# Performance work log

Hardware: AMD Instinct MI355X
Metric: run time of the kernel (lower is better)

Reference implementation:

```python
import jax, jax.numpy as jnp
import numpy as np

NUM_HEADS = 2
DIM_NODE = 100
DIM_EDGE = 100
DIM_TIME = 100
DIM_OUT = 100
N_DST = 32768
N_EDGE = 524288
LN_EPS = 1e-5


def setup_inputs() -> dict:
    key = jax.random.key(0)
    ks = jax.random.split(key, 12)
    dst_h = jax.random.normal(ks[0], (N_DST, DIM_NODE), dtype=jnp.float32)
    src_h = jax.random.normal(ks[1], (N_EDGE, DIM_NODE), dtype=jnp.float32)
    efeat = jax.random.normal(ks[2], (N_EDGE, DIM_EDGE), dtype=jnp.float32)
    # time deltas are non-negative elapsed times
    time_deltas = jax.random.uniform(ks[3], (N_EDGE,), dtype=jnp.float32) * 1000.0
    edge_dst = jnp.sort(jax.random.randint(ks[4], (N_EDGE,), 0, N_DST, dtype=jnp.int32))
    # TimeEncode: fixed geometric frequencies, zero bias
    time_w = jnp.asarray(1.0 / 10 ** np.linspace(0, 9, DIM_TIME), dtype=jnp.float32)
    time_b = jnp.zeros((DIM_TIME,), dtype=jnp.float32)
    def lin(k, fan_out, fan_in):
        s = 1.0 / np.sqrt(fan_in)
        return jax.random.uniform(k, (fan_out, fan_in), jnp.float32, -s, s)
    wq_w = lin(ks[5], DIM_OUT, DIM_NODE + DIM_TIME)
    wq_b = jax.random.normal(ks[6], (DIM_OUT,), jnp.float32) * 0.02
    wkv_w = lin(ks[7], 2 * DIM_OUT, DIM_NODE + DIM_EDGE + DIM_TIME)
    wkv_b = jax.random.normal(ks[8], (2 * DIM_OUT,), jnp.float32) * 0.02
    wout_w = lin(ks[9], DIM_OUT, DIM_NODE + DIM_OUT)
    wout_b = jax.random.normal(ks[10], (DIM_OUT,), jnp.float32) * 0.02
    ln_g = jnp.ones((DIM_OUT,), jnp.float32)
    ln_b = jnp.zeros((DIM_OUT,), jnp.float32)
    return dict(dst_h=dst_h, src_h=src_h, efeat=efeat, time_deltas=time_deltas,
                edge_dst=edge_dst, time_w=time_w, time_b=time_b,
                wq_w=wq_w, wq_b=wq_b, wkv_w=wkv_w, wkv_b=wkv_b,
                wout_w=wout_w, wout_b=wout_b, ln_g=ln_g, ln_b=ln_b)


def reference(dst_h, src_h, efeat, time_deltas, edge_dst, time_w, time_b,
              wq_w, wq_b, wkv_w, wkv_b, wout_w, wout_b, ln_g, ln_b):
    n_dst = dst_h.shape[0]
    dim_out = wq_w.shape[0]
    dh = dim_out // NUM_HEADS
    # TimeEncode: cos(w*t + b); zero-time feature for dst nodes
    zero_tf = jnp.broadcast_to(jnp.cos(time_b), (n_dst, time_b.shape[0]))
    nbr_tf = jnp.cos(time_deltas[:, None] * time_w[None, :] + time_b)  # [E, dim_time]
    Q = jnp.concatenate([dst_h, zero_tf], axis=1) @ wq_w.T + wq_b       # [N_dst, dim_out]
    Z = jnp.concatenate([src_h, efeat, nbr_tf], axis=1) @ wkv_w.T + wkv_b  # [E, 2*dim_out]
    K = Z[:, :dim_out].reshape(-1, NUM_HEADS, dh)
    V = Z[:, dim_out:].reshape(-1, NUM_HEADS, dh)
    Qe = Q[edge_dst].reshape(-1, NUM_HEADS, dh)  # edge_view gather
    attn = jnp.sum(Qe * K, axis=2)               # [E, H]
    attn = jax.nn.leaky_relu(attn, negative_slope=0.2)
    # edge_softmax: segment softmax over edges grouped by dst
    m = jax.ops.segment_max(attn, edge_dst, num_segments=n_dst)
    e = jnp.exp(attn - m[edge_dst])
    s = jax.ops.segment_sum(e, edge_dst, num_segments=n_dst)
    a = e / s[edge_dst]                           # [E, H]
    out_e = (V * a[:, :, None]).reshape(-1, dim_out)
    out = jax.ops.segment_sum(out_e, edge_dst, num_segments=n_dst)  # edge_reduce sum
    out = jnp.concatenate([out, dst_h], axis=1) @ wout_w.T + wout_b
    out = jax.nn.relu(out)  # dropout disabled (eval)
    mu = jnp.mean(out, axis=-1, keepdims=True)
    var = jnp.var(out, axis=-1, keepdims=True)
    return (out - mu) / jnp.sqrt(var + LN_EPS) * ln_g + ln_b
```

## Files before the change

### kernel.cpp

```cpp
#include <hip/hip_runtime.h>
#include <math.h>

#define N_DST   32768
#define N_EDGE  524288
#define LN_EPS  1e-5f

typedef __attribute__((ext_vector_type(8))) short short8b;
typedef __attribute__((ext_vector_type(4))) float f32x4;

static __device__ __forceinline__ unsigned short f2bf(float f) {
    unsigned u = __float_as_uint(f);
    u += 0x7fff + ((u >> 16) & 1);
    return (unsigned short)(u >> 16);
}

__global__ void k_prep(const float* __restrict__ wkv_w, const float* __restrict__ wq_w,
                       const float* __restrict__ wq_b, const float* __restrict__ time_b,
                       const float* __restrict__ wout_w,
                       float* __restrict__ zq, float* __restrict__ wout_t,
                       unsigned short* __restrict__ Bv) {
    int idx = blockIdx.x * 256 + threadIdx.x;
    if (idx < 100) {
        float acc = wq_b[idx];
        for (int j = 0; j < 100; ++j)
            acc += cosf(time_b[j]) * wq_w[idx * 200 + 100 + j];
        zq[idx] = acc;
    } else if (idx < 20100) {
        int r = idx - 100;
        wout_t[r] = wout_w[(size_t)(r % 100) * 200 + r / 100];
    } else if (idx < 95364) {
        int r2 = idx - 20100;
        int jj = r2 & 7, l = (r2 >> 3) & 63, nf = (r2 >> 9) % 7, kc = r2 / 3584;
        int j = kc * 32 + ((l >> 4) << 3) + jj;
        int o = nf * 16 + (l & 15);
        float v = (j < 600 && o < 100 && (j / 300 == o / 50))
                  ? wkv_w[(size_t)(100 + o) * 300 + (j % 300)] : 0.f;
        Bv[r2] = f2bf(v);
    }
}

__global__ void k_precomp(const float* __restrict__ wq_w, const float* __restrict__ wkv_w,
                          const float* __restrict__ wkv_b, const float* __restrict__ zq,
                          float* __restrict__ A2, float* __restrict__ C2) {
    int idx = blockIdx.x * 256 + threadIdx.x;
    if (idx < 60200) {
        int i = idx / 602, j = idx % 602;
        float acc = 0.f;
        if (j < 600) {
            int h = j / 300, cc = j % 300;
            const float* __restrict__ wq = wq_w + (size_t)(h * 50) * 200 + i;
            const float* __restrict__ wk = wkv_w + (size_t)(h * 50) * 300 + cc;
            #pragma unroll 10
            for (int d = 0; d < 50; ++d)
                acc = fmaf(wq[(size_t)d * 200], wk[(size_t)d * 300], acc);
        } else {
            int h = j - 600;
            const float* __restrict__ wq = wq_w + (size_t)(h * 50) * 200 + i;
            for (int d = 0; d < 50; ++d)
                acc = fmaf(wq[(size_t)d * 200], wkv_b[h * 50 + d], acc);
        }
        A2[idx] = acc;
    } else if (idx < 60802) {
        int j = idx - 60200;
        float acc = 0.f;
        if (j < 600) {
            int h = j / 300, cc = j % 300;
            for (int d = 0; d < 50; ++d)
                acc = fmaf(zq[h * 50 + d], wkv_w[(size_t)(h * 50 + d) * 300 + cc], acc);
        } else {
            int h = j - 600;
            for (int d = 0; d < 50; ++d)
                acc = fmaf(zq[h * 50 + d], wkv_b[h * 50 + d], acc);
        }
        C2[j] = acc;
    }
}

__global__ void k_pack(const float* __restrict__ A2, unsigned short* __restrict__ Bq) {
    int idx = blockIdx.x * 256 + threadIdx.x;
    if (idx >= 77824) return;
    int jj = idx & 7, l = (idx >> 3) & 63, nf = (idx >> 9) % 19, kcp = idx / 9728;
    int kc = kcp & 3, p = kcp >> 2;
    int k = kc * 32 + ((l >> 4) << 3) + jj;
    int c = p * 304 + nf * 16 + (l & 15);
    float v = (k < 100 && c < 602) ? A2[(size_t)k * 602 + c] : 0.f;
    Bq[idx] = f2bf(v);
}

__global__ void k_offsets(const int* __restrict__ dst, int* __restrict__ off) {
    int n = blockIdx.x * 256 + threadIdx.x;
    if (n > N_DST) return;
    int lo = 0, hi = N_EDGE;
    while (lo < hi) {
        int mid = (lo + hi) >> 1;
        if (dst[mid] < n) lo = mid + 1; else hi = mid;
    }
    off[n] = lo;
}

__global__ __launch_bounds__(256, 1) void k_qw(
        const float* __restrict__ dst_h, const unsigned short* __restrict__ Bq,
        const float* __restrict__ C2, float* __restrict__ QW) {
    __shared__ alignas(16) unsigned short Bs[9728];
    const int t = threadIdx.x, lane = t & 63;
    const int g = blockIdx.x * 4 + (t >> 6);
    const int col = lane & 15, slice = lane >> 4;
    const int row = g * 16 + col;

    short8b af[4];
    {
        const float* __restrict__ dr = dst_h + (size_t)row * 100;
        #pragma unroll
        for (int kc = 0; kc < 4; ++kc) {
            int k0 = kc * 32 + slice * 8;
            float4 xa = make_float4(0.f, 0.f, 0.f, 0.f), xb = xa;
            if (k0 + 8 <= 100) { xa = *(const float4*)(dr + k0); xb = *(const float4*)(dr + k0 + 4); }
            else if (k0 < 100)  { xa = *(const float4*)(dr + k0); }
            short8b a;
            a[0] = (short)f2bf(xa.x); a[1] = (short)f2bf(xa.y);
            a[2] = (short)f2bf(xa.z); a[3] = (short)f2bf(xa.w);
            a[4] = (short)f2bf(xb.x); a[5] = (short)f2bf(xb.y);
            a[6] = (short)f2bf(xb.z); a[7] = (short)f2bf(xb.w);
            af[kc] = a;
        }
    }
    const int re0 = g * 16 + (slice << 2);
    #pragma unroll
    for (int p = 0; p < 2; ++p) {
        f32x4 acc[19];
        #pragma unroll
        for (int nf = 0; nf < 19; ++nf) {
            int c = p * 304 + nf * 16 + col;
            float b = (c < 602) ? C2[c] : 0.f;
            acc[nf] = (f32x4){b, b, b, b};
        }
        #pragma unroll
        for (int kc = 0; kc < 4; ++kc) {
            {
                const float4* __restrict__ ws4 = (const float4*)Bq + (size_t)(p * 4 + kc) * 1216;
                float4* __restrict__ wd = (float4*)Bs;
                #pragma unroll
                for (int i = 0; i < 4; ++i) wd[i * 256 + t] = ws4[i * 256 + t];
                if (t < 192) wd[1024 + t] = ws4[1024 + t];
            }
            __syncthreads();
            #pragma unroll
            for (int nf = 0; nf < 19; ++nf) {
                short8b w = *(const short8b*)(&Bs[(size_t)(nf * 64 + lane) * 8]);
                acc[nf] = __builtin_amdgcn_mfma_f32_16x16x32_bf16(af[kc], w, acc[nf], 0, 0, 0);
            }
            __syncthreads();
        }
        #pragma unroll
        for (int nf = 0; nf < 19; ++nf) {
            int c = p * 304 + nf * 16 + col;
            if (c < 602) {
                #pragma unroll
                for (int r = 0; r < 4; ++r)
                    QW[(size_t)(re0 + r) * 608 + c] = acc[nf][r];
            }
        }
    }
}

__global__ __launch_bounds__(256) void k_node(
        const float* __restrict__ src_h, const float* __restrict__ efeat,
        const float* __restrict__ td,
        const float* __restrict__ time_w, const float* __restrict__ time_b,
        const float* __restrict__ QW, const int* __restrict__ off,
        float* __restrict__ Xagg) {
    const int lane = threadIdx.x & 63;
    const int n = blockIdx.x * 4 + (threadIdx.x >> 6);
    const int r0 = off[n], cnt = off[n + 1] - r0;
    float* __restrict__ xo = Xagg + (size_t)n * 600;
    if (cnt <= 0) {
        #pragma unroll
        for (int s = 0; s < 5; ++s) {
            int cc = s * 64 + lane;
            if (cc < 300) { xo[cc] = 0.f; xo[300 + cc] = 0.f; }
        }
        return;
    }
    float qw0[5], qw1[5];
    #pragma unroll
    for (int s = 0; s < 5; ++s) {
        int cc = s * 64 + lane;
        qw0[s] = (cc < 300) ? QW[(size_t)n * 608 + cc]       : 0.f;
        qw1[s] = (cc < 300) ? QW[(size_t)n * 608 + 300 + cc] : 0.f;
    }
    const float B0 = QW[(size_t)n * 608 + 600];
    const float B1 = QW[(size_t)n * 608 + 601];
    float tw3 = 0.f, tb3 = 0.f, tw4 = 0.f, tb4 = 0.f;
    if (lane >= 8) { tw3 = time_w[lane - 8]; tb3 = time_b[lane - 8]; }
    if (lane < 44) { tw4 = time_w[56 + lane]; tb4 = time_b[56 + lane]; }

    auto LOADX = [&](float* x, int r) {
        const float* __restrict__ sr = src_h + (size_t)r * 100;
        const float* __restrict__ er = efeat + (size_t)r * 100;
        const float tdv = td[r];
        x[0] = sr[lane];
        x[1] = (lane < 36) ? sr[64 + lane] : er[lane - 36];
        x[2] = er[28 + lane];
        x[3] = (lane < 8) ? er[92 + lane] : __cosf(fmaf(tdv, tw3, tb3));
        x[4] = (lane < 44) ? __cosf(fmaf(tdv, tw4, tb4)) : 0.f;
    };

    float m0 = -1e30f, m1 = -1e30f, sum0 = 0.f, sum1 = 0.f;
    float a0[5] = {0.f, 0.f, 0.f, 0.f, 0.f}, a1[5] = {0.f, 0.f, 0.f, 0.f, 0.f};

    auto UPDATE = [&](float l0, float l1, const float* x) {
        l0 = l0 > 0.f ? l0 : 0.2f * l0;
        l1 = l1 > 0.f ? l1 : 0.2f * l1;
        if (l0 <= m0 && l1 <= m1) {
            float w0 = __expf(l0 - m0), w1 = __expf(l1 - m1);
            sum0 += w0; sum1 += w1;
            #pragma unroll
            for (int s = 0; s < 5; ++s) {
                a0[s] = fmaf(w0, x[s], a0[s]);
                a1[s] = fmaf(w1, x[s], a1[s]);
            }
        } else {
            float m0n = fmaxf(m0, l0), m1n = fmaxf(m1, l1);
            float r0f = __expf(m0 - m0n), r1f = __expf(m1 - m1n);
            float w0 = __expf(l0 - m0n),  w1 = __expf(l1 - m1n);
            sum0 = fmaf(sum0, r0f, w0);
            sum1 = fmaf(sum1, r1f, w1);
            #pragma unroll
            for (int s = 0; s < 5; ++s) {
                a0[s] = fmaf(a0[s], r0f, w0 * x[s]);
                a1[s] = fmaf(a1[s], r1f, w1 * x[s]);
            }
            m0 = m0n; m1 = m1n;
        }
    };

    float xA[5], xB[5], xC[5], xD[5];
    int i = 0;
    if (cnt >= 2) {
        LOADX(xA, r0); LOADX(xB, r0 + 1);
        for (; i + 2 <= cnt; i += 2) {
            float pA0 = 0.f, pA1 = 0.f, pB0 = 0.f, pB1 = 0.f;
            #pragma unroll
            for (int s = 0; s < 5; ++s) {
                pA0 = fmaf(xA[s], qw0[s], pA0); pA1 = fmaf(xA[s], qw1[s], pA1);
                pB0 = fmaf(xB[s], qw0[s], pB0); pB1 = fmaf(xB[s], qw1[s], pB1);
            }
            #pragma unroll
            for (int sh = 1; sh < 64; sh <<= 1) {
                pA0 += __shfl_xor(pA0, sh); pA1 += __shfl_xor(pA1, sh);
                pB0 += __shfl_xor(pB0, sh); pB1 += __shfl_xor(pB1, sh);
            }
            if (i + 2 < cnt) LOADX(xC, r0 + i + 2);
            if (i + 3 < cnt) LOADX(xD, r0 + i + 3);
            UPDATE(pA0 + B0, pA1 + B1, xA);
            UPDATE(pB0 + B0, pB1 + B1, xB);
            #pragma unroll
            for (int s = 0; s < 5; ++s) { xA[s] = xC[s]; xB[s] = xD[s]; }
        }
    } else {
        LOADX(xA, r0);
    }
    if (i < cnt) {
        float p0 = 0.f, p1 = 0.f;
        #pragma unroll
        for (int s = 0; s < 5; ++s) {
            p0 = fmaf(xA[s], qw0[s], p0);
            p1 = fmaf(xA[s], qw1[s], p1);
        }
        #pragma unroll
        for (int sh = 1; sh < 64; sh <<= 1) {
            p0 += __shfl_xor(p0, sh); p1 += __shfl_xor(p1, sh);
        }
        UPDATE(p0 + B0, p1 + B1, xA);
    }
    const float inv0 = 1.f / sum0, inv1 = 1.f / sum1;
    #pragma unroll
    for (int s = 0; s < 5; ++s) {
        int cc = s * 64 + lane;
        if (cc < 300) {
            xo[cc]       = a0[s] * inv0;
            xo[300 + cc] = a1[s] * inv1;
        }
    }
}

__global__ __launch_bounds__(256, 1) void k_aggv(
        const float* __restrict__ Xagg, const unsigned short* __restrict__ Bv,
        const float* __restrict__ wkv_b, const int* __restrict__ off,
        float* __restrict__ agg) {
    __shared__ alignas(16) unsigned short Bs[10752];
    const int t = threadIdx.x, lane = t & 63;
    const int g = blockIdx.x * 4 + (t >> 6);
    const int col = lane & 15, slice = lane >> 4;
    const int row = g * 16 + col;

    short8b af[21];
    {
        const float* __restrict__ xr = Xagg + (size_t)row * 600;
        #pragma unroll
        for (int kc = 0; kc < 21; ++kc) {
            int j0 = kc * 32 + slice * 8;
            float4 xa = make_float4(0.f, 0.f, 0.f, 0.f), xb = xa;
            if (j0 + 8 <= 600) { xa = *(const float4*)(xr + j0); xb = *(const float4*)(xr + j0 + 4); }
            short8b a;
            a[0] = (short)f2bf(xa.x); a[1] = (short)f2bf(xa.y);
            a[2] = (short)f2bf(xa.z); a[3] = (short)f2bf(xa.w);
            a[4] = (short)f2bf(xb.x); a[5] = (short)f2bf(xb.y);
            a[6] = (short)f2bf(xb.z); a[7] = (short)f2bf(xb.w);
            af[kc] = a;
        }
    }
    f32x4 acc[7];
    #pragma unroll
    for (int nf = 0; nf < 7; ++nf) acc[nf] = (f32x4){0.f, 0.f, 0.f, 0.f};

    #pragma unroll
    for (int slab = 0; slab < 7; ++slab) {
        {
            const float4* __restrict__ ws4 = (const float4*)Bv + (size_t)slab * 1344;
            float4* __restrict__ wd = (float4*)Bs;
            #pragma unroll
            for (int i = 0; i < 5; ++i) wd[i * 256 + t] = ws4[i * 256 + t];
            if (t < 64) wd[1280 + t] = ws4[1280 + t];
        }
        __syncthreads();
        #pragma unroll
        for (int kl = 0; kl < 3; ++kl) {
            const int kc = slab * 3 + kl;
            #pragma unroll
            for (int nf = 0; nf < 7; ++nf) {
                short8b w = *(const short8b*)(&Bs[(size_t)((kl * 7 + nf) * 64 + lane) * 8]);
                acc[nf] = __builtin_amdgcn_mfma_f32_16x16x32_bf16(af[kc], w, acc[nf], 0, 0, 0);
            }
        }
        __syncthreads();
    }
    const int re0 = g * 16 + (slice << 2);
    #pragma unroll
    for (int nf = 0; nf < 7; ++nf) {
        int o = nf * 16 + col;
        if (o < 100) {
            float bv = wkv_b[100 + o];
            #pragma unroll
            for (int r = 0; r < 4; ++r) {
                int node = re0 + r;
                bool has = off[node + 1] > off[node];
                agg[(size_t)node * 100 + o] = acc[nf][r] + (has ? bv : 0.f);
            }
        }
    }
}

__global__ __launch_bounds__(128) void k_out(const float* __restrict__ agg,
                                             const float* __restrict__ dst_h,
                                             const float* __restrict__ wout_t,
                                             const float* __restrict__ wout_b,
                                             const float* __restrict__ ln_g,
                                             const float* __restrict__ ln_b,
                                             float* __restrict__ out) {
    __shared__ float Fs[8][200];
    __shared__ float red[8][128];
    const int n0 = blockIdx.x * 8, t = threadIdx.x;
    for (int idx = t; idx < 1600; idx += 128) {
        int n = idx / 200, i = idx % 200;
        Fs[n][i] = (i < 100) ? agg[(size_t)(n0 + n) * 100 + i]
                             : dst_h[(size_t)(n0 + n) * 100 + (i - 100)];
    }
    __syncthreads();
    float v[8] = {0.f, 0.f, 0.f, 0.f, 0.f, 0.f, 0.f, 0.f};
    if (t < 100) {
        float b = wout_b[t];
        #pragma unroll
        for (int n = 0; n < 8; ++n) v[n] = b;
        for (int i = 0; i < 200; ++i) {
            float w = wout_t[i * 100 + t];
            #pragma unroll
            for (int n = 0; n < 8; ++n) v[n] = fmaf(Fs[n][i], w, v[n]);
        }
        #pragma unroll
        for (int n = 0; n < 8; ++n) v[n] = fmaxf(v[n], 0.f);
    }
    #pragma unroll
    for (int n = 0; n < 8; ++n) red[n][t] = (t < 100) ? v[n] : 0.f;
    __syncthreads();
    for (int s = 64; s > 0; s >>= 1) {
        if (t < s) {
            #pragma unroll
            for (int n = 0; n < 8; ++n) red[n][t] += red[n][t + s];
        }
        __syncthreads();
    }
    float mu[8];
    #pragma unroll
    for (int n = 0; n < 8; ++n) mu[n] = red[n][0] * 0.01f;
    __syncthreads();
    #pragma unroll
    for (int n = 0; n < 8; ++n) {
        float dv = (t < 100) ? (v[n] - mu[n]) : 0.f;
        red[n][t] = dv * dv;
    }
    __syncthreads();
    for (int s = 64; s > 0; s >>= 1) {
        if (t < s) {
            #pragma unroll
            for (int n = 0; n < 8; ++n) red[n][t] += red[n][t + s];
        }
        __syncthreads();
    }
    if (t < 100) {
        #pragma unroll
        for (int n = 0; n < 8; ++n) {
            float var = red[n][0] * 0.01f;
            out[(size_t)(n0 + n) * 100 + t] =
                (v[n] - mu[n]) * rsqrtf(var + LN_EPS) * ln_g[t] + ln_b[t];
        }
    }
}

extern "C" void kernel_launch(void* const* d_in, const int* in_sizes, int n_in,
                              void* d_out, int out_size, void* d_ws, size_t ws_size,
                              hipStream_t stream) {
    const float* dst_h   = (const float*)d_in[0];
    const float* src_h   = (const float*)d_in[1];
    const float* efeat   = (const float*)d_in[2];
    const float* td      = (const float*)d_in[3];
    const int*   edst    = (const int*)  d_in[4];
    const float* time_w  = (const float*)d_in[5];
    const float* time_b  = (const float*)d_in[6];
    const float* wq_w    = (const float*)d_in[7];
    const float* wq_b    = (const float*)d_in[8];
    const float* wkv_w   = (const float*)d_in[9];
    const float* wkv_b   = (const float*)d_in[10];
    const float* wout_w  = (const float*)d_in[11];
    const float* wout_b  = (const float*)d_in[12];
    const float* ln_g    = (const float*)d_in[13];
    const float* ln_b    = (const float*)d_in[14];
    float* out = (float*)d_out;

    char* ws = (char*)d_ws;
    size_t off = 0;
    auto carve = [&](size_t bytes) { char* p = ws + off; off = (off + bytes + 255) & ~(size_t)255; return p; };
    float*          QW    = (float*)carve((size_t)N_DST * 608 * 4);
    float*          Xagg  = (float*)carve((size_t)N_DST * 600 * 4);
    float*          agg   = (float*)carve((size_t)N_DST * 100 * 4);
    float*          A2    = (float*)carve(60200 * 4);
    float*          C2    = (float*)carve(602 * 4);
    unsigned short* Bq    = (unsigned short*)carve(77824 * 2);
    unsigned short* Bv    = (unsigned short*)carve(75264 * 2);
    float*          woutT = (float*)carve(20000 * 4);
    float*          zq    = (float*)carve(100 * 4);
    int*            offs  = (int*)carve((size_t)(N_DST + 1) * 4);

    k_prep<<<(95364 + 255) / 256, 256, 0, stream>>>(wkv_w, wq_w, wq_b, time_b, wout_w,
                                                    zq, woutT, Bv);
    k_precomp<<<(60802 + 255) / 256, 256, 0, stream>>>(wq_w, wkv_w, wkv_b, zq, A2, C2);
    k_pack<<<(77824 + 255) / 256, 256, 0, stream>>>(A2, Bq);
    k_offsets<<<(N_DST + 1 + 255) / 256, 256, 0, stream>>>(edst, offs);
    k_qw<<<N_DST / 64, 256, 0, stream>>>(dst_h, Bq, C2, QW);
    k_node<<<N_DST / 4, 256, 0, stream>>>(src_h, efeat, td, time_w, time_b,
                                          QW, offs, Xagg);
    k_aggv<<<N_DST / 64, 256, 0, stream>>>(Xagg, Bv, wkv_b, offs, agg);
    k_out<<<N_DST / 8, 128, 0, stream>>>(agg, dst_h, woutT, wout_b, ln_g, ln_b, out);
}
```

Measured before the change: 327.2 us.

## Split each node's edges across two wavefronts and merge softmax partials in LDS

k_node now assigns two wavefronts per destination node, each handling alternating edges with its own online-softmax state. The second wave's partial max, sum and weighted accumulators go through shared memory, and the first wave merges them with rescaling before writing Xagg. This shortens the serial per-node edge chain (about 16 edges on average) to expose more memory-level parallelism. In exchange it adds a block barrier, LDS traffic, and double the per-node QW loads.

```diff
diff --git a/kernel.cpp b/kernel.cpp
--- a/kernel.cpp
+++ b/kernel.cpp
@@ -169,117 +169,147 @@
         const float* __restrict__ time_w, const float* __restrict__ time_b,
         const float* __restrict__ QW, const int* __restrict__ off,
         float* __restrict__ Xagg) {
-    const int lane = threadIdx.x & 63;
-    const int n = blockIdx.x * 4 + (threadIdx.x >> 6);
+    const int t = threadIdx.x, lane = t & 63;
+    const int ns = t >> 7;
+    const int sub = (t >> 6) & 1;
+    const int n = blockIdx.x * 2 + ns;
+    __shared__ float Pa[2][64][10];
+    __shared__ float Pm[2][4];
     const int r0 = off[n], cnt = off[n + 1] - r0;
-    float* __restrict__ xo = Xagg + (size_t)n * 600;
-    if (cnt <= 0) {
+
+    float m0 = -1e30f, m1 = -1e30f, sum0 = 0.f, sum1 = 0.f;
+    float a0[5] = {0.f, 0.f, 0.f, 0.f, 0.f}, a1[5] = {0.f, 0.f, 0.f, 0.f, 0.f};
+
+    if (cnt > 0) {
+        float qw0[5], qw1[5];
         #pragma unroll
         for (int s = 0; s < 5; ++s) {
             int cc = s * 64 + lane;
-            if (cc < 300) { xo[cc] = 0.f; xo[300 + cc] = 0.f; }
-        }
-        return;
-    }
-    float qw0[5], qw1[5];
-    #pragma unroll
-    for (int s = 0; s < 5; ++s) {
-        int cc = s * 64 + lane;
-        qw0[s] = (cc < 300) ? QW[(size_t)n * 608 + cc]       : 0.f;
-        qw1[s] = (cc < 300) ? QW[(size_t)n * 608 + 300 + cc] : 0.f;
-    }
-    const float B0 = QW[(size_t)n * 608 + 600];
-    const float B1 = QW[(size_t)n * 608 + 601];
-    float tw3 = 0.f, tb3 = 0.f, tw4 = 0.f, tb4 = 0.f;
-    if (lane >= 8) { tw3 = time_w[lane - 8]; tb3 = time_b[lane - 8]; }
-    if (lane < 44) { tw4 = time_w[56 + lane]; tb4 = time_b[56 + lane]; }
-
-    auto LOADX = [&](float* x, int r) {
-        const float* __restrict__ sr = src_h + (size_t)r * 100;
-        const float* __restrict__ er = efeat + (size_t)r * 100;
-        const float tdv = td[r];
-        x[0] = sr[lane];
-        x[1] = (lane < 36) ? sr[64 + lane] : er[lane - 36];
-        x[2] = er[28 + lane];
-        x[3] = (lane < 8) ? er[92 + lane] : __cosf(fmaf(tdv, tw3, tb3));
-        x[4] = (lane < 44) ? __cosf(fmaf(tdv, tw4, tb4)) : 0.f;
-    };
-
-    float m0 = -1e30f, m1 = -1e30f, sum0 = 0.f, sum1 = 0.f;
-    float a0[5] = {0.f, 0.f, 0.f, 0.f, 0.f}, a1[5] = {0.f, 0.f, 0.f, 0.f, 0.f};
-
-    auto UPDATE = [&](float l0, float l1, const float* x) {
-        l0 = l0 > 0.f ? l0 : 0.2f * l0;
-        l1 = l1 > 0.f ? l1 : 0.2f * l1;
-        if (l0 <= m0 && l1 <= m1) {
-            float w0 = __expf(l0 - m0), w1 = __expf(l1 - m1);
-            sum0 += w0; sum1 += w1;
+            qw0[s] = (cc < 300) ? QW[(size_t)n * 608 + cc]       : 0.f;
+            qw1[s] = (cc < 300) ? QW[(size_t)n * 608 + 300 + cc] : 0.f;
+        }
+        const float B0 = QW[(size_t)n * 608 + 600];
+        const float B1 = QW[(size_t)n * 608 + 601];
+        float tw3 = 0.f, tb3 = 0.f, tw4 = 0.f, tb4 = 0.f;
+        if (lane >= 8) { tw3 = time_w[lane - 8]; tb3 = time_b[lane - 8]; }
+        if (lane < 44) { tw4 = time_w[56 + lane]; tb4 = time_b[56 + lane]; }
+
+        auto LOADX = [&](float* x, int r) {
+            const float* __restrict__ sr = src_h + (size_t)r * 100;
+            const float* __restrict__ er = efeat + (size_t)r * 100;
+            const float tdv = td[r];
+            x[0] = sr[lane];
+            x[1] = (lane < 36) ? sr[64 + lane] : er[lane - 36];
+            x[2] = er[28 + lane];
+            x[3] = (lane < 8) ? er[92 + lane] : __cosf(fmaf(tdv, tw3, tb3));
+            x[4] = (lane < 44) ? __cosf(fmaf(tdv, tw4, tb4)) : 0.f;
+        };
+
+        auto UPDATE = [&](float l0, float l1, const float* x) {
+            l0 = l0 > 0.f ? l0 : 0.2f * l0;
+            l1 = l1 > 0.f ? l1 : 0.2f * l1;
+            if (l0 <= m0 && l1 <= m1) {
+                float w0 = __expf(l0 - m0), w1 = __expf(l1 - m1);
+                sum0 += w0; sum1 += w1;
+                #pragma unroll
+                for (int s = 0; s < 5; ++s) {
+                    a0[s] = fmaf(w0, x[s], a0[s]);
+                    a1[s] = fmaf(w1, x[s], a1[s]);
+                }
+            } else {
+                float m0n = fmaxf(m0, l0), m1n = fmaxf(m1, l1);
+                float r0f = __expf(m0 - m0n), r1f = __expf(m1 - m1n);
+                float w0 = __expf(l0 - m0n),  w1 = __expf(l1 - m1n);
+                sum0 = fmaf(sum0, r0f, w0);
+                sum1 = fmaf(sum1, r1f, w1);
+                #pragma unroll
+                for (int s = 0; s < 5; ++s) {
+                    a0[s] = fmaf(a0[s], r0f, w0 * x[s]);
+                    a1[s] = fmaf(a1[s], r1f, w1 * x[s]);
+                }
+                m0 = m0n; m1 = m1n;
+            }
+        };
+
+        const int nloc = (cnt - sub + 1) >> 1;
+        auto IDX = [&](int k) { return r0 + sub + 2 * k; };
+        float xA[5], xB[5], xC[5], xD[5];
+        int k = 0;
+        if (nloc >= 2) {
+            LOADX(xA, IDX(0)); LOADX(xB, IDX(1));
+            for (; k + 2 <= nloc; k += 2) {
+                float pA0 = 0.f, pA1 = 0.f, pB0 = 0.f, pB1 = 0.f;
+                #pragma unroll
+                for (int s = 0; s < 5; ++s) {
+                    pA0 = fmaf(xA[s], qw0[s], pA0); pA1 = fmaf(xA[s], qw1[s], pA1);
+                    pB0 = fmaf(xB[s], qw0[s], pB0); pB1 = fmaf(xB[s], qw1[s], pB1);
+                }
+                #pragma unroll
+                for (int sh = 1; sh < 64; sh <<= 1) {
+                    pA0 += __shfl_xor(pA0, sh); pA1 += __shfl_xor(pA1, sh);
+                    pB0 += __shfl_xor(pB0, sh); pB1 += __shfl_xor(pB1, sh);
+                }
+                if (k + 2 < nloc) LOADX(xC, IDX(k + 2));
+                if (k + 3 < nloc) LOADX(xD, IDX(k + 3));
+                UPDATE(pA0 + B0, pA1 + B1, xA);
+                UPDATE(pB0 + B0, pB1 + B1, xB);
+                #pragma unroll
+                for (int s = 0; s < 5; ++s) { xA[s] = xC[s]; xB[s] = xD[s]; }
+            }
+        } else if (nloc == 1) {
+            LOADX(xA, IDX(0));
+        }
+        if (k < nloc) {
+            float p0 = 0.f, p1 = 0.f;
             #pragma unroll
             for (int s = 0; s < 5; ++s) {
-                a0[s] = fmaf(w0, x[s], a0[s]);
-                a1[s] = fmaf(w1, x[s], a1[s]);
+                p0 = fmaf(xA[s], qw0[s], p0);
+                p1 = fmaf(xA[s], qw1[s], p1);
+            }
+            #pragma unroll
+            for (int sh = 1; sh < 64; sh <<= 1) {
+                p0 += __shfl_xor(p0, sh); p1 += __shfl_xor(p1, sh);
+            }
+            UPDATE(p0 + B0, p1 + B1, xA);
+        }
+    }
+
+    if (sub == 1) {
+        #pragma unroll
+        for (int s = 0; s < 5; ++s) {
+            Pa[ns][lane][s]     = a0[s];
+            Pa[ns][lane][5 + s] = a1[s];
+        }
+        if (lane == 0) {
+            Pm[ns][0] = m0; Pm[ns][1] = m1; Pm[ns][2] = sum0; Pm[ns][3] = sum1;
+        }
+    }
+    __syncthreads();
+    if (sub == 0) {
+        float* __restrict__ xo = Xagg + (size_t)n * 600;
+        if (cnt <= 0) {
+            #pragma unroll
+            for (int s = 0; s < 5; ++s) {
+                int cc = s * 64 + lane;
+                if (cc < 300) { xo[cc] = 0.f; xo[300 + cc] = 0.f; }
             }
         } else {
-            float m0n = fmaxf(m0, l0), m1n = fmaxf(m1, l1);
-            float r0f = __expf(m0 - m0n), r1f = __expf(m1 - m1n);
-            float w0 = __expf(l0 - m0n),  w1 = __expf(l1 - m1n);
-            sum0 = fmaf(sum0, r0f, w0);
-            sum1 = fmaf(sum1, r1f, w1);
+            float mb0 = Pm[ns][0], mb1 = Pm[ns][1], sb0 = Pm[ns][2], sb1 = Pm[ns][3];
+            float M0 = fmaxf(m0, mb0), M1 = fmaxf(m1, mb1);
+            float fa0 = __expf(m0 - M0), fb0 = __expf(mb0 - M0);
+            float fa1 = __expf(m1 - M1), fb1 = __expf(mb1 - M1);
+            float inv0 = 1.f / fmaf(sb0, fb0, sum0 * fa0);
+            float inv1 = 1.f / fmaf(sb1, fb1, sum1 * fa1);
             #pragma unroll
             for (int s = 0; s < 5; ++s) {
-                a0[s] = fmaf(a0[s], r0f, w0 * x[s]);
-                a1[s] = fmaf(a1[s], r1f, w1 * x[s]);
-            }
-            m0 = m0n; m1 = m1n;
-        }
-    };
-
-    float xA[5], xB[5], xC[5], xD[5];
-    int i = 0;
-    if (cnt >= 2) {
-        LOADX(xA, r0); LOADX(xB, r0 + 1);
-        for (; i + 2 <= cnt; i += 2) {
-            float pA0 = 0.f, pA1 = 0.f, pB0 = 0.f, pB1 = 0.f;
-            #pragma unroll
-            for (int s = 0; s < 5; ++s) {
-                pA0 = fmaf(xA[s], qw0[s], pA0); pA1 = fmaf(xA[s], qw1[s], pA1);
-                pB0 = fmaf(xB[s], qw0[s], pB0); pB1 = fmaf(xB[s], qw1[s], pB1);
-            }
-            #pragma unroll
-            for (int sh = 1; sh < 64; sh <<= 1) {
-                pA0 += __shfl_xor(pA0, sh); pA1 += __shfl_xor(pA1, sh);
-                pB0 += __shfl_xor(pB0, sh); pB1 += __shfl_xor(pB1, sh);
-            }
-            if (i + 2 < cnt) LOADX(xC, r0 + i + 2);
-            if (i + 3 < cnt) LOADX(xD, r0 + i + 3);
-            UPDATE(pA0 + B0, pA1 + B1, xA);
-            UPDATE(pB0 + B0, pB1 + B1, xB);
-            #pragma unroll
-            for (int s = 0; s < 5; ++s) { xA[s] = xC[s]; xB[s] = xD[s]; }
-        }
-    } else {
-        LOADX(xA, r0);
-    }
-    if (i < cnt) {
-        float p0 = 0.f, p1 = 0.f;
-        #pragma unroll
-        for (int s = 0; s < 5; ++s) {
-            p0 = fmaf(xA[s], qw0[s], p0);
-            p1 = fmaf(xA[s], qw1[s], p1);
-        }
-        #pragma unroll
-        for (int sh = 1; sh < 64; sh <<= 1) {
-            p0 += __shfl_xor(p0, sh); p1 += __shfl_xor(p1, sh);
-        }
-        UPDATE(p0 + B0, p1 + B1, xA);
-    }
-    const float inv0 = 1.f / sum0, inv1 = 1.f / sum1;
-    #pragma unroll
-    for (int s = 0; s < 5; ++s) {
-        int cc = s * 64 + lane;
-        if (cc < 300) {
-            xo[cc]       = a0[s] * inv0;
-            xo[300 + cc] = a1[s] * inv1;
+                int cc = s * 64 + lane;
+                if (cc < 300) {
+                    float v0 = fmaf(Pa[ns][lane][s],     fb0, a0[s] * fa0);
+                    float v1 = fmaf(Pa[ns][lane][5 + s], fb1, a1[s] * fa1);
+                    xo[cc]       = v0 * inv0;
+                    xo[300 + cc] = v1 * inv1;
+                }
+            }
         }
     }
 }
@@ -457,7 +487,7 @@
     k_pack<<<(77824 + 255) / 256, 256, 0, stream>>>(A2, Bq);
     k_offsets<<<(N_DST + 1 + 255) / 256, 256, 0, stream>>>(edst, offs);
     k_qw<<<N_DST / 64, 256, 0, stream>>>(dst_h, Bq, C2, QW);
-    k_node<<<N_DST / 4, 256, 0, stream>>>(src_h, efeat, td, time_w, time_b,
+    k_node<<<N_DST / 2, 256, 0, stream>>>(src_h, efeat, td, time_w, time_b,
                                           QW, offs, Xagg);
     k_aggv<<<N_DST / 64, 256, 0, stream>>>(Xagg, Bv, wkv_b, offs, agg);
     k_out<<<N_DST / 8, 128, 0, stream>>>(agg, dst_h, woutT, wout_b, ln_g, ln_b, out);
```

Result: slower. 339.6 us (+3.8%).
